# Kernel tuning notes

Hardware: AMD Instinct MI355X
Metric: run time of the kernel (lower is better)

The kernel has to match this reference:

```python
import jax, jax.numpy as jnp
import numpy as np

PAD_VALUE = 0.0
DUR_MAX = 8  # exclusive upper bound on per-phoneme duration -> static padded length T*DUR_MAX


def setup_inputs() -> dict:
    key = jax.random.key(0)
    k1, k2 = jax.random.split(key)
    B, T, D = 32, 512, 384
    xs = jax.random.normal(k1, (B, T, D), dtype=jnp.float32)
    durations = jax.random.randint(k2, (B, T), 0, DUR_MAX, dtype=jnp.int32)
    return {"xs": xs, "durations": durations}


def reference(xs, durations):
    # xs: [B, T, D] phoneme embeddings; durations: [B, T] frames per phoneme.
    # Expands each phoneme embedding `duration` times along time, left-aligned,
    # padded with PAD_VALUE to a static max frame length T*DUR_MAX (jit-safe
    # upper bound on the data-dependent max length used by the torch module).
    B, T, D = xs.shape
    T_out = T * DUR_MAX

    d = durations
    # torch edge case: if ALL durations are zero, rows with zero total get 1s.
    total = d.sum()
    row_sum = d.sum(axis=1)
    d = jnp.where((total == 0) & (row_sum == 0)[:, None], 1, d)

    cum = jnp.cumsum(d, axis=1)                      # [B, T] exclusive->inclusive frame offsets
    t = jnp.arange(T_out, dtype=cum.dtype)           # [T_out]
    # frame t belongs to phoneme j where cum[j-1] <= t < cum[j]
    idx = jax.vmap(lambda c: jnp.searchsorted(c, t, side="right"))(cum)  # [B, T_out]
    valid = t[None, :] < cum[:, -1][:, None]         # [B, T_out]
    idx = jnp.minimum(idx, T - 1)                    # clamp for safe gather

    out = jnp.take_along_axis(xs, idx[:, :, None], axis=1)  # [B, T_out, D]
    return jnp.where(valid[:, :, None], out, jnp.asarray(PAD_VALUE, xs.dtype))
```

## Files before the change

### kernel.cpp

```cpp
#include <hip/hip_runtime.h>
#include <hip/hip_bf16.h>


#define B   32
#define T   512
#define D   384
#define TOUT 4096
#define CH  (D / 4)
#define F   64

__global__ __launch_bounds__(256) void k_total(const int* __restrict__ dur,
                                               int* __restrict__ flag) {
    __shared__ int ssum[4];
    int tid = threadIdx.x;
    int sum = 0;
    for (int i = tid; i < B * T; i += 256) sum += dur[i];
    #pragma unroll
    for (int o = 32; o > 0; o >>= 1) sum += __shfl_down(sum, o);
    if ((tid & 63) == 0) ssum[tid >> 6] = sum;
    __syncthreads();
    if (tid == 0) {
        int tot = ssum[0] + ssum[1] + ssum[2] + ssum[3];
        flag[0] = (tot == 0) ? 1 : 0;
    }
}

__global__ __launch_bounds__(512) void k_scan(const int* __restrict__ dur,
                                              const int* __restrict__ flag,
                                              int* __restrict__ cum) {
    __shared__ int s[T];
    int b = blockIdx.x, t = threadIdx.x;
    int d = dur[b * T + t];
    if (flag[0]) d = 1;
    s[t] = d;
    __syncthreads();
    #pragma unroll
    for (int off = 1; off < T; off <<= 1) {
        int v = (t >= off) ? s[t - off] : 0;
        __syncthreads();
        s[t] += v;
        __syncthreads();
    }
    cum[b * T + t] = s[t];
}

__global__ __launch_bounds__(256) void k_expand(const float4* __restrict__ xs4,
                                                const int* __restrict__ cum,
                                                float4* __restrict__ out4) {
    __shared__ int s_cum[T];
    __shared__ int s_idx[F];
    const int b = blockIdx.y;
    const int frame0 = blockIdx.x * F;
    const int tid = threadIdx.x;

    for (int i = tid; i < T; i += 256) s_cum[i] = cum[b * T + i];
    __syncthreads();

    const int last = s_cum[T - 1];
    if (tid < F) {
        int t = frame0 + tid;
        int idx = 0;
        #pragma unroll
        for (int step = T / 2; step > 0; step >>= 1)
            if (s_cum[idx + step - 1] <= t) idx += step;
        if (idx > T - 1) idx = T - 1;
        s_idx[tid] = (t < last) ? idx : -1;
    }
    __syncthreads();

    #pragma unroll 4
    for (int item = tid; item < F * CH; item += 256) {
        int f = item / CH;
        int c = item - f * CH;
        int j = s_idx[f];
        float4 v = make_float4(0.f, 0.f, 0.f, 0.f);
        if (j >= 0) v = xs4[(b * T + j) * CH + c];
        out4[((size_t)b * TOUT + frame0 + f) * CH + c] = v;
    }
}

extern "C" void kernel_launch(void* const* d_in, const int* in_sizes, int n_in,
                              void* d_out, int out_size, void* d_ws, size_t ws_size,
                              hipStream_t stream) {
    const float* xs  = (const float*)d_in[0];
    const int*   dur = (const int*)d_in[1];
    float*       out = (float*)d_out;

    int* flag = (int*)d_ws;
    int* cum  = (int*)((char*)d_ws + 64);

    k_total<<<1, 256, 0, stream>>>(dur, flag);
    k_scan<<<B, T, 0, stream>>>(dur, flag, cum);
    dim3 grid(TOUT / F, B);
    k_expand<<<grid, 256, 0, stream>>>((const float4*)xs, cum, (float4*)out);
}
```

Measured before the change: 245.3 us.

## Fuse total check, scan and expand into one length-regulator kernel

Merges the three launches (global zero-sum flag, per-row scan, expand) into a single kernel. Each block redoes its row's prefix scan in shared memory and only scans all durations when its own row sums to zero. Frames per block go from 64 to 128 and threads from 256 to 512. This removes two launches and the workspace round trip, at the price of every block repeating the row scan.

```diff
diff --git a/kernel.cpp b/kernel.cpp
--- a/kernel.cpp
+++ b/kernel.cpp
@@ -2,59 +2,47 @@
 #include <hip/hip_bf16.h>
 
 
-#define B   32
-#define T   512
-#define D   384
+#define B    32
+#define T    512
+#define D    384
 #define TOUT 4096
-#define CH  (D / 4)
-#define F   64
+#define CH   (D / 4)
+#define F    128
+#define NT   512
 
-__global__ __launch_bounds__(256) void k_total(const int* __restrict__ dur,
-                                               int* __restrict__ flag) {
-    __shared__ int ssum[4];
-    int tid = threadIdx.x;
-    int sum = 0;
-    for (int i = tid; i < B * T; i += 256) sum += dur[i];
-    #pragma unroll
-    for (int o = 32; o > 0; o >>= 1) sum += __shfl_down(sum, o);
-    if ((tid & 63) == 0) ssum[tid >> 6] = sum;
-    __syncthreads();
-    if (tid == 0) {
-        int tot = ssum[0] + ssum[1] + ssum[2] + ssum[3];
-        flag[0] = (tot == 0) ? 1 : 0;
-    }
-}
+__global__ __launch_bounds__(NT) void k_lenreg(const float4* __restrict__ xs4,
+                                               const int* __restrict__ dur,
+                                               float4* __restrict__ out4) {
+    __shared__ int s_cum[T];
+    __shared__ int s_idx[F];
+    __shared__ int s_red[NT / 64];
+    const int b      = blockIdx.y;
+    const int frame0 = blockIdx.x * F;
+    const int tid    = threadIdx.x;
 
-__global__ __launch_bounds__(512) void k_scan(const int* __restrict__ dur,
-                                              const int* __restrict__ flag,
-                                              int* __restrict__ cum) {
-    __shared__ int s[T];
-    int b = blockIdx.x, t = threadIdx.x;
-    int d = dur[b * T + t];
-    if (flag[0]) d = 1;
-    s[t] = d;
+    s_cum[tid] = dur[b * T + tid];
     __syncthreads();
     #pragma unroll
     for (int off = 1; off < T; off <<= 1) {
-        int v = (t >= off) ? s[t - off] : 0;
+        int v = (tid >= off) ? s_cum[tid - off] : 0;
         __syncthreads();
-        s[t] += v;
+        s_cum[tid] += v;
         __syncthreads();
     }
-    cum[b * T + t] = s[t];
-}
 
-__global__ __launch_bounds__(256) void k_expand(const float4* __restrict__ xs4,
-                                                const int* __restrict__ cum,
-                                                float4* __restrict__ out4) {
-    __shared__ int s_cum[T];
-    __shared__ int s_idx[F];
-    const int b = blockIdx.y;
-    const int frame0 = blockIdx.x * F;
-    const int tid = threadIdx.x;
-
-    for (int i = tid; i < T; i += 256) s_cum[i] = cum[b * T + i];
-    __syncthreads();
+    if (s_cum[T - 1] == 0) {
+        int sum = 0;
+        for (int i = tid; i < B * T; i += NT) sum += dur[i];
+        #pragma unroll
+        for (int o = 32; o > 0; o >>= 1) sum += __shfl_down(sum, o);
+        if ((tid & 63) == 0) s_red[tid >> 6] = sum;
+        __syncthreads();
+        int tot = 0;
+        #pragma unroll
+        for (int w = 0; w < NT / 64; ++w) tot += s_red[w];
+        if (tot == 0) s_cum[tid] = tid + 1;
+        __syncthreads();
+    }
 
     const int last = s_cum[T - 1];
     if (tid < F) {
@@ -68,14 +56,16 @@
     }
     __syncthreads();
 
+    const size_t obase = ((size_t)b * TOUT + frame0) * CH;
+    const size_t ibase = (size_t)b * T * CH;
     #pragma unroll 4
-    for (int item = tid; item < F * CH; item += 256) {
+    for (int item = tid; item < F * CH; item += NT) {
         int f = item / CH;
         int c = item - f * CH;
         int j = s_idx[f];
         float4 v = make_float4(0.f, 0.f, 0.f, 0.f);
-        if (j >= 0) v = xs4[(b * T + j) * CH + c];
-        out4[((size_t)b * TOUT + frame0 + f) * CH + c] = v;
+        if (j >= 0) v = xs4[ibase + (size_t)j * CH + c];
+        out4[obase + item] = v;
     }
 }
 
@@ -86,11 +76,6 @@
     const int*   dur = (const int*)d_in[1];
     float*       out = (float*)d_out;
 
-    int* flag = (int*)d_ws;
-    int* cum  = (int*)((char*)d_ws + 64);
-
-    k_total<<<1, 256, 0, stream>>>(dur, flag);
-    k_scan<<<B, T, 0, stream>>>(dur, flag, cum);
     dim3 grid(TOUT / F, B);
-    k_expand<<<grid, 256, 0, stream>>>((const float4*)xs, cum, (float4*)out);
+    k_lenreg<<<grid, NT, 0, stream>>>((const float4*)xs, dur, (float4*)out);
 }
```

New measurement: 228.2 us. 1.07x faster.
